# Kernel optimization log

Hardware: AMD Instinct MI355X
Metric: run time of the kernel (lower is better)

The kernel has to match this reference:

```python
import jax, jax.numpy as jnp
import numpy as np

EPS = 1e-12  # matches torch F.normalize eps

def _l2norm(x, axis):
    n = jnp.sqrt(jnp.sum(x * x, axis=axis, keepdims=True))
    return x / jnp.maximum(n, EPS)

def setup_inputs() -> dict:
    key = jax.random.key(0)
    b, N, c, h, w = 8, 4, 256, 64, 64
    n, hw, L = N - 1, h * w, 2048
    k1, k2, k3, k4, k5 = jax.random.split(key, 5)
    feat = jax.random.normal(k1, (b, c, h, w), dtype=jnp.float32)
    refs = jax.random.normal(k2, (b, N, c, h, w), dtype=jnp.float32)
    similarity = jax.random.uniform(k3, (b, N), dtype=jnp.float32)
    # unique indices per row (the torch code pads by repeating mask indices; we use
    # unique ones so the final scatter is deterministic)
    base_indices = jax.vmap(lambda k: jax.random.permutation(k, hw))(jax.random.split(k4, b))[:, :L].astype(jnp.int64)
    ref_idx = jax.vmap(lambda k: jax.random.permutation(k, hw))(jax.random.split(k5, b * n))
    ref_indices_in = ref_idx.reshape(b, n, hw)[:, :, :L].astype(jnp.int64)
    return {"feat": feat, "refs": refs, "similarity": similarity,
            "base_indices": base_indices, "ref_indices_in": ref_indices_in, "index": 0}

def reference(feat, refs, similarity, base_indices, ref_indices_in, index):
    b, N, c, h, w = refs.shape
    n, hw = N - 1, h * w
    L = base_indices.shape[1]
    # drop the base reference slot
    refs_r = jnp.concatenate([refs[:, :index], refs[:, index + 1:]], axis=1)      # [b,n,c,h,w]
    base_sim = similarity[:, index]                                              # [b]
    ref_sims = jnp.concatenate([similarity[:, :index], similarity[:, index + 1:]], axis=1)  # [b,n]

    feat_flat = feat.reshape(b, c, hw)                                           # [b,c,hw]
    w_feat = _l2norm(feat_flat.transpose(0, 2, 1), axis=2)                       # [b,hw,c]
    w_refs = _l2norm(refs_r.reshape(b, n, c, hw), axis=2)                        # [b,n,c,hw]

    # gather masked positions
    feat_select = jnp.take_along_axis(feat_flat, base_indices[:, None, :], axis=2)      # [b,c,L]
    w_feat_sel = _l2norm(jnp.take_along_axis(w_feat, base_indices[:, :, None], axis=1), axis=2)  # [b,L,c]
    w_ref_sel = jnp.take_along_axis(w_refs, ref_indices_in[:, :, None, :], axis=3)      # [b,n,c,L]

    # cosine similarity + top-1 match per base position, per reference
    fx = jnp.einsum('blc,bncm->bnlm', w_feat_sel, w_ref_sel)                     # [b,n,L,L]
    ref_indices = jnp.argmax(fx, axis=3)                                         # [b,n,L] (top-1)
    ref_selects = jnp.take_along_axis(w_ref_sel, ref_indices[:, :, None, :], axis=3)    # [b,n,c,L]

    # similarity-weighted fusion
    feat_fused = base_sim[:, None, None] * feat_select \
               + jnp.einsum('bn,bncl->bcl', ref_sims, ref_selects)               # [b,c,L]

    # scatter fused features back into the base feature map
    bi = jnp.arange(b)[:, None, None]
    ci = jnp.arange(c)[None, :, None]
    out = feat_flat.at[bi, ci, base_indices[:, None, :]].set(feat_fused)
    return out.reshape(b, c, h, w), base_indices, ref_indices
```

## Files before the change

kernel.cpp:

```cpp
#include <hip/hip_runtime.h>
#include <math.h>

#define HWp 4096
#define Cp 256
#define Lp 2048
#define Np 3
#define Bp 8

#define OUT_FEAT_N 8388608
#define OUT_BASE_OFF 8388608
#define OUT_REF_OFF 8404992
#define NROWS 49152

#define OFF_AF16  ((size_t)0)
#define OFF_BF16  ((size_t)16777216)
#define OFF_PVAL  ((size_t)117440512)
#define OFF_BEST  ((size_t)119799808)
#define OFF_CAND2 ((size_t)119996416)
#define OFF_COUNT ((size_t)120193024)
#define OFF_LIST  ((size_t)120193280)
#define OFF_INV   ((size_t)120389888)

typedef _Float16 f16x8 __attribute__((ext_vector_type(8)));
typedef float f32x4 __attribute__((ext_vector_type(4)));

__device__ __forceinline__ unsigned short f16bits(float x){
    union { _Float16 h; unsigned short s; } u;
    u.h = (_Float16)x;
    return u.s;
}

__global__ void init_inv_kernel(int4* __restrict__ inv4){
    int tid = blockIdx.x * blockDim.x + threadIdx.x;
    if (tid < 32768) inv4[tid] = make_int4(-1, -1, -1, -1);
}

__global__ void scatter_inv_kernel(const int* __restrict__ refIdxI,
                                   const int* __restrict__ baseIdx,
                                   int* __restrict__ inv){
    int tid = blockIdx.x * blockDim.x + threadIdx.x;
    if (tid < NROWS){
        int g = tid >> 11;
        inv[g*4096 + refIdxI[tid]] = tid & 2047;
    } else if (tid < NROWS + Bp*Lp){
        int t = tid - NROWS;
        int b = t >> 11;
        inv[(24 + b)*4096 + baseIdx[t]] = t & 2047;
    }
}

__global__ __launch_bounds__(256) void gather_kernel(
    const float* __restrict__ feat, const float* __restrict__ refs,
    const int* __restrict__ pindex, const int* __restrict__ inv,
    unsigned char* __restrict__ Af16, unsigned char* __restrict__ Bf16)
{
    int tileh = blockIdx.x & 127;
    int g = blockIdx.x >> 7;
    int isRef = (g < 24);
    const float* src;
    int b;
    if (isRef){
        b = g / 3; int r0 = g - b*3; int iv = *pindex;
        int rn = (r0 < iv) ? r0 : r0 + 1;
        src = refs + ((size_t)(b*4 + rn)) * Cp * HWp;
    } else {
        b = g - 24;
        src = feat + (size_t)b * Cp * HWp;
    }
    __shared__ float lds[32 * 256];
    __shared__ float ssqp[4][32];
    __shared__ float rinv[32];
    int tid = threadIdx.x, hwl = tid & 31, cg = tid >> 5;
    int hw0 = tileh * 32;
    const float* sp = src + hw0 + hwl;
    int swz = hwl << 2;
    float* lrow = lds + hwl * 256;
    float ss = 0.f;
    #pragma unroll
    for (int i = 0; i < 8; i++){
        int c0 = cg * 32 + i * 4;
        float x0 = sp[(size_t)(c0 + 0) * HWp];
        float x1 = sp[(size_t)(c0 + 1) * HWp];
        float x2 = sp[(size_t)(c0 + 2) * HWp];
        float x3 = sp[(size_t)(c0 + 3) * HWp];
        ss = fmaf(x0, x0, fmaf(x1, x1, fmaf(x2, x2, fmaf(x3, x3, ss))));
        *(float4*)(lrow + (c0 ^ swz)) = make_float4(x0, x1, x2, x3);
    }
    ss += __shfl_xor(ss, 32, 64);
    int w = tid >> 6, lane = tid & 63;
    if (lane < 32) ssqp[w][lane] = ss;
    __syncthreads();
    if (tid < 32){
        float s = ssqp[0][tid] + ssqp[1][tid] + ssqp[2][tid] + ssqp[3][tid];
        rinv[tid] = 1.0f / fmaxf(sqrtf(s), 1e-12f);
    }
    __syncthreads();
    const int* invg = inv + g * 4096 + hw0;
    unsigned char* dstBase = isRef ? (Bf16 + (size_t)g * Lp * 512)
                                   : (Af16 + (size_t)b * Lp * 512);
    for (int h = w * 8; h < w * 8 + 8; h++){
        int dest = invg[h];
        if (dest < 0) continue;
        float4 v = *(float4*)(lds + h * 256 + ((lane * 4) ^ (h << 2)));
        float rn = rinv[h];
        ushort4 hv;
        hv.x = f16bits(v.x * rn); hv.y = f16bits(v.y * rn);
        hv.z = f16bits(v.z * rn); hv.w = f16bits(v.w * rn);
        *(ushort4*)(dstBase + (size_t)dest * 512 + lane * 8) = hv;
    }
}

__device__ __forceinline__ void stage4(const unsigned char* srcLane, unsigned char* ldsW){
    #pragma unroll
    for (int p = 0; p < 4; p++)
        __builtin_amdgcn_global_load_lds(
            (const __attribute__((address_space(1))) void*)(srcLane + (p & 1) * 8192 + (p >> 1) * 64),
            (__attribute__((address_space(3))) void*)(ldsW + p * 1024),
            16, 0, 0);
}

__global__ __launch_bounds__(256, 3) void gemm_mfma_kernel(
    const unsigned char* __restrict__ Af16, const unsigned char* __restrict__ Bf16,
    unsigned int* __restrict__ ppk)
{
    int orig = (blockIdx.x & 7) * 192 + (blockIdx.x >> 3);
    int rowgrp = orig & 15;
    int chunk = (orig >> 4) % 12;
    int b = orig / 192;
    int n = chunk >> 2, c4 = chunk & 3;
    int bn = b*3 + n;
    int tid = threadIdx.x, lane = tid & 63, w = tid >> 6;
    int l15 = lane & 15, lg = lane >> 4;

    __shared__ unsigned char bufs[2][16384];

    int row0 = rowgrp*128 + w*16 + l15;
    const unsigned char* Arow0 = Af16 + ((size_t)b*Lp + row0)*512 + lg*16;
    const unsigned char* Arow1 = Arow0 + (size_t)64*512;
    f16x8 A0[8], A1[8];
    #pragma unroll
    for (int ks = 0; ks < 8; ks++){
        A0[ks] = *(const f16x8*)(Arow0 + ks*64);
        A1[ks] = *(const f16x8*)(Arow1 + ks*64);
    }

    unsigned p1[8], p2[8];
    #pragma unroll
    for (int s = 0; s < 8; s++){ p1[s] = 0u; p2[s] = 0u; }

    const unsigned char* srcLane = Bf16
        + ((size_t)(bn*2048 + c4*512)) * 512
        + l15 * 512 + (lane >> 4) * 16 + w * 128;
    unsigned char* ldsW0 = &bufs[0][w*4096];
    unsigned char* ldsW1 = &bufs[1][w*4096];

    stage4(srcLane, ldsW0);

    #pragma unroll 1
    for (int t = 0; t < 16; t++){
        if (t < 15){
            stage4(srcLane + (size_t)(t+1)*16384, (t & 1) ? ldsW0 : ldsW1);
            asm volatile("s_waitcnt vmcnt(4)" ::: "memory");
        } else {
            asm volatile("s_waitcnt vmcnt(0)" ::: "memory");
        }
        __builtin_amdgcn_s_barrier();

        const unsigned char* bp = bufs[t & 1];
        f32x4 a00 = {2.f,2.f,2.f,2.f}, a01 = {2.f,2.f,2.f,2.f};
        f32x4 a10 = {2.f,2.f,2.f,2.f}, a11 = {2.f,2.f,2.f,2.f};
        #pragma unroll
        for (int ks = 0; ks < 8; ks++){
            f16x8 b0 = *(const f16x8*)(bp + ks*2048 + lane*16);
            f16x8 b1 = *(const f16x8*)(bp + ks*2048 + 1024 + lane*16);
            a00 = __builtin_amdgcn_mfma_f32_16x16x32_f16(A0[ks], b0, a00, 0, 0, 0);
            a01 = __builtin_amdgcn_mfma_f32_16x16x32_f16(A0[ks], b1, a01, 0, 0, 0);
            a10 = __builtin_amdgcn_mfma_f32_16x16x32_f16(A1[ks], b0, a10, 0, 0, 0);
            a11 = __builtin_amdgcn_mfma_f32_16x16x32_f16(A1[ks], b1, a11, 0, 0, 0);
        }
        __builtin_amdgcn_s_barrier();

        unsigned ci0 = (unsigned)(511 - (t*32 + l15));
        unsigned ci1 = ci0 - 16;
        #pragma unroll
        for (int r = 0; r < 4; r++){
            {
                unsigned u0 = (__float_as_uint(a00[r]) & 0xFFFFFE00u) | ci0;
                unsigned u1 = (__float_as_uint(a01[r]) & 0xFFFFFE00u) | ci1;
                unsigned hi = max(u0, u1), lo = min(u0, u1);
                unsigned tm = min(p1[r], hi);
                p1[r] = max(p1[r], hi);
                p2[r] = max(p2[r], max(lo, tm));
            }
            {
                unsigned u0 = (__float_as_uint(a10[r]) & 0xFFFFFE00u) | ci0;
                unsigned u1 = (__float_as_uint(a11[r]) & 0xFFFFFE00u) | ci1;
                unsigned hi = max(u0, u1), lo = min(u0, u1);
                unsigned tm = min(p1[4+r], hi);
                p1[4+r] = max(p1[4+r], hi);
                p2[4+r] = max(p2[4+r], max(lo, tm));
            }
        }
    }

    #pragma unroll
    for (int s = 0; s < 8; s++){
        unsigned q1 = p1[s], q2 = p2[s];
        #pragma unroll
        for (int off = 1; off < 16; off <<= 1){
            unsigned o1 = (unsigned)__shfl_xor((int)q1, off, 64);
            unsigned o2 = (unsigned)__shfl_xor((int)q2, off, 64);
            unsigned m1 = max(q1, o1);
            unsigned m2 = max(min(q1, o1), max(q2, o2));
            q1 = m1; q2 = m2;
        }
        if (l15 == 0){
            int rs = s >> 2, r = s & 3;
            size_t grow = (size_t)bn*Lp + rowgrp*128 + rs*64 + w*16 + lg*4 + r;
            size_t slot = grow*4 + c4;
            ppk[slot*2 + 0] = q1;
            ppk[slot*2 + 1] = q2;
        }
    }
}

__global__ void reset_kernel(int* count){ *count = 0; }

__global__ void combine_kernel(const unsigned int* __restrict__ ppk,
                               int* __restrict__ best, int* __restrict__ cand2,
                               float* __restrict__ outF, const int* __restrict__ baseIdx,
                               int* __restrict__ count, int* __restrict__ list)
{
    int gid = blockIdx.x * blockDim.x + threadIdx.x;
    if (gid < NROWS){
        unsigned V1 = 0u, V2 = 0u; int X1 = 0, X2 = 0;
        #pragma unroll
        for (int ch = 0; ch < 4; ch++){
            unsigned u1 = ppk[((size_t)gid*4 + ch)*2 + 0];
            unsigned u2 = ppk[((size_t)gid*4 + ch)*2 + 1];
            unsigned vb1 = u1 & 0xFFFFFE00u; int c1 = ch*512 + 511 - (int)(u1 & 511u);
            unsigned vb2 = u2 & 0xFFFFFE00u; int c2 = ch*512 + 511 - (int)(u2 & 511u);
            if (vb1 > V1 || (vb1 == V1 && c1 < X1)){
                V2 = V1; X2 = X1; V1 = vb1; X1 = c1;
            } else if (vb1 > V2 || (vb1 == V2 && c1 < X2)){
                V2 = vb1; X2 = c1;
            }
            if (vb2 > V2 || (vb2 == V2 && c2 < X2)){ V2 = vb2; X2 = c2; }
        }
        best[gid] = X1; cand2[gid] = X2;
        outF[OUT_REF_OFF + gid] = (float)X1;
        if (__uint_as_float(V1) - __uint_as_float(V2) < 3.6e-4f){
            int s = atomicAdd(count, 1);
            if (s < NROWS) list[s] = gid;
        }
    }
    if (gid < Bp*Lp) outF[OUT_BASE_OFF + gid] = (float)baseIdx[gid];
}

__global__ void refine_kernel(const float* __restrict__ feat, const float* __restrict__ refs,
                              const int* __restrict__ baseIdx, const int* __restrict__ refIdxI,
                              const int* __restrict__ pindex,
                              const int* __restrict__ count, const int* __restrict__ list,
                              int* __restrict__ best, const int* __restrict__ cand2,
                              float* __restrict__ outF)
{
    int nf = *count; if (nf > NROWS) nf = NROWS;
    int lane = threadIdx.x & 63;
    int iv = *pindex;
    for (int it = blockIdx.x; it < nf; it += gridDim.x){
        int gid = list[it];
        int bn = gid >> 11, l = gid & 2047;
        int b = bn / 3; int r0 = bn - b*3;
        int rn = (r0 < iv) ? r0 : r0 + 1;
        int i1 = best[gid], i2 = cand2[gid];
        int posA = baseIdx[b*Lp + l];
        int pos1 = refIdxI[bn*Lp + i1];
        int pos2 = refIdxI[bn*Lp + i2];
        const float* fA = feat + (size_t)b * Cp * HWp + posA;
        const float* fR = refs + (size_t)(b*4 + rn) * Cp * HWp;
        const float* f1 = fR + pos1;
        const float* f2 = fR + pos2;
        double s1 = 0, s2 = 0, d1 = 0, d2 = 0;
        #pragma unroll
        for (int j = 0; j < 4; j++){
            int c = lane * 4 + j;
            double a  = (double)fA[(size_t)c * HWp];
            double x1 = (double)f1[(size_t)c * HWp];
            double x2 = (double)f2[(size_t)c * HWp];
            s1 += x1*x1; s2 += x2*x2;
            d1 += a*x1;  d2 += a*x2;
        }
        #pragma unroll
        for (int off = 1; off < 64; off <<= 1){
            s1 += __shfl_xor(s1, off, 64);
            s2 += __shfl_xor(s2, off, 64);
            d1 += __shfl_xor(d1, off, 64);
            d2 += __shfl_xor(d2, off, 64);
        }
        if (lane == 0){
            double q1 = d1 * sqrt(s2), q2 = d2 * sqrt(s1);
            int ix = (q2 > q1 || (q2 == q1 && i2 < i1)) ? i2 : i1;
            best[gid] = ix;
            outF[OUT_REF_OFF + gid] = (float)ix;
        }
    }
}

__global__ __launch_bounds__(256) void fuse_tile_kernel(
    const float* __restrict__ feat, const unsigned char* __restrict__ Bf16,
    const int* __restrict__ best, const int* __restrict__ inv,
    const float* __restrict__ sim, const int* __restrict__ pindex,
    float* __restrict__ out)
{
    int tileh = blockIdx.x & 63;
    int b = blockIdx.x >> 6;
    int hw0 = tileh * 64;
    __shared__ float lds[256 * 64];
    int tid = threadIdx.x, hwl = tid & 63, cg = tid >> 6;
    const float* fb = feat + (size_t)b * Cp * HWp + hw0 + hwl;
    #pragma unroll 4
    for (int i = 0; i < 64; i++){
        int c = cg * 64 + i;
        lds[c * 64 + ((hwl + c) & 63)] = fb[(size_t)c * HWp];
    }
    __syncthreads();
    int iv = *pindex;
    float bs  = sim[b*4 + iv];
    float rs0 = sim[b*4 + ((0 < iv) ? 0 : 1)];
    float rs1 = sim[b*4 + ((1 < iv) ? 1 : 2)];
    float rs2 = sim[b*4 + ((2 < iv) ? 2 : 3)];
    int w = cg, lane = tid & 63;
    const int* invg = inv + (24 + b) * 4096 + hw0;
    for (int h = w * 16; h < w * 16 + 16; h++){
        int dest = invg[h];
        if (dest < 0) continue;
        int b0 = best[(b*3 + 0)*Lp + dest];
        int b1 = best[(b*3 + 1)*Lp + dest];
        int b2 = best[(b*3 + 2)*Lp + dest];
        const unsigned char* r0 = Bf16 + ((size_t)(b*3 + 0)*Lp + b0) * 512;
        const unsigned char* r1 = Bf16 + ((size_t)(b*3 + 1)*Lp + b1) * 512;
        const unsigned char* r2 = Bf16 + ((size_t)(b*3 + 2)*Lp + b2) * 512;
        #pragma unroll
        for (int j = 0; j < 4; j++){
            int c = lane + j * 64;
            int la = c * 64 + ((h + c) & 63);
            float base = lds[la];
            float v0 = (float)(*(const _Float16*)(r0 + c*2));
            float v1 = (float)(*(const _Float16*)(r1 + c*2));
            float v2 = (float)(*(const _Float16*)(r2 + c*2));
            lds[la] = bs*base + rs0*v0 + rs1*v1 + rs2*v2;
        }
    }
    __syncthreads();
    float* ob = out + (size_t)b * Cp * HWp + hw0 + hwl;
    #pragma unroll 4
    for (int i = 0; i < 64; i++){
        int c = cg * 64 + i;
        ob[(size_t)c * HWp] = lds[c * 64 + ((hwl + c) & 63)];
    }
}

extern "C" void kernel_launch(void* const* d_in, const int* in_sizes, int n_in,
                              void* d_out, int out_size, void* d_ws, size_t ws_size,
                              hipStream_t stream)
{
    const float* feat    = (const float*)d_in[0];
    const float* refs    = (const float*)d_in[1];
    const float* sim     = (const float*)d_in[2];
    const int*   baseIdx = (const int*)d_in[3];
    const int*   refIdxI = (const int*)d_in[4];
    const int*   pindex  = (const int*)d_in[5];
    float* out = (float*)d_out;
    unsigned char* ws = (unsigned char*)d_ws;

    unsigned char* Af16 = ws + OFF_AF16;
    unsigned char* Bf16 = ws + OFF_BF16;
    unsigned int* ppk = (unsigned int*)(ws + OFF_PVAL);
    int* best  = (int*)(ws + OFF_BEST);
    int* cand2 = (int*)(ws + OFF_CAND2);
    int* count = (int*)(ws + OFF_COUNT);
    int* list  = (int*)(ws + OFF_LIST);
    int* inv   = (int*)(ws + OFF_INV);

    init_inv_kernel<<<128, 256, 0, stream>>>((int4*)inv);
    scatter_inv_kernel<<<256, 256, 0, stream>>>(refIdxI, baseIdx, inv);
    gather_kernel<<<4096, 256, 0, stream>>>(feat, refs, pindex, inv, Af16, Bf16);
    gemm_mfma_kernel<<<1536, 256, 0, stream>>>(Af16, Bf16, ppk);
    reset_kernel<<<1, 1, 0, stream>>>(count);
    combine_kernel<<<192, 256, 0, stream>>>(ppk, best, cand2, out, baseIdx, count, list);
    refine_kernel<<<512, 64, 0, stream>>>(feat, refs, baseIdx, refIdxI, pindex, count, list, best, cand2, out);
    fuse_tile_kernel<<<512, 256, 0, stream>>>(feat, Bf16, best, inv, sim, pindex, out);
}
```

Before: 153.3 us.

## Halve LDS staging per step to raise GEMM occupancy with split-K halves

Splits each 32-column B tile's K dimension into two half-steps, staging 8KB instead of 16KB of LDS per buffer. Launch bounds go from 3 to 6 blocks per CU. Partial accumulators from the first half are saved in registers and added to the second half before the packed top-2 update. The aim is more resident waves to hide load latency, at the cost of twice as many barriers and waits, extra live registers under a tighter register budget, and a slightly different float summation order.

```diff
diff --git a/kernel.cpp b/kernel.cpp
--- a/kernel.cpp
+++ b/kernel.cpp
@@ -110,16 +110,16 @@
     }
 }
 
-__device__ __forceinline__ void stage4(const unsigned char* srcLane, unsigned char* ldsW){
+__device__ __forceinline__ void stage2(const unsigned char* srcLane, unsigned char* ldsW){
     #pragma unroll
-    for (int p = 0; p < 4; p++)
+    for (int p = 0; p < 2; p++)
         __builtin_amdgcn_global_load_lds(
-            (const __attribute__((address_space(1))) void*)(srcLane + (p & 1) * 8192 + (p >> 1) * 64),
+            (const __attribute__((address_space(1))) void*)(srcLane + p * 8192),
             (__attribute__((address_space(3))) void*)(ldsW + p * 1024),
             16, 0, 0);
 }
 
-__global__ __launch_bounds__(256, 3) void gemm_mfma_kernel(
+__global__ __launch_bounds__(256, 6) void gemm_mfma_kernel(
     const unsigned char* __restrict__ Af16, const unsigned char* __restrict__ Bf16,
     unsigned int* __restrict__ ppk)
 {
@@ -132,7 +132,7 @@
     int tid = threadIdx.x, lane = tid & 63, w = tid >> 6;
     int l15 = lane & 15, lg = lane >> 4;
 
-    __shared__ unsigned char bufs[2][16384];
+    __shared__ unsigned char bufs[2][8192];
 
     int row0 = rowgrp*128 + w*16 + l15;
     const unsigned char* Arow0 = Af16 + ((size_t)b*Lp + row0)*512 + lg*16;
@@ -150,29 +150,33 @@
 
     const unsigned char* srcLane = Bf16
         + ((size_t)(bn*2048 + c4*512)) * 512
-        + l15 * 512 + (lane >> 4) * 16 + w * 128;
-    unsigned char* ldsW0 = &bufs[0][w*4096];
-    unsigned char* ldsW1 = &bufs[1][w*4096];
-
-    stage4(srcLane, ldsW0);
+        + l15 * 512 + (lane >> 4) * 16 + w * 64;
+
+    f32x4 sv00, sv01, sv10, sv11;
+
+    stage2(srcLane, &bufs[0][w*2048]);
 
     #pragma unroll 1
-    for (int t = 0; t < 16; t++){
-        if (t < 15){
-            stage4(srcLane + (size_t)(t+1)*16384, (t & 1) ? ldsW0 : ldsW1);
-            asm volatile("s_waitcnt vmcnt(4)" ::: "memory");
+    for (int q = 0; q < 32; q++){
+        if (q < 31){
+            int t1 = (q + 1) >> 1, h1 = (q + 1) & 1;
+            stage2(srcLane + (size_t)t1*16384 + (size_t)h1*256,
+                   &bufs[(q+1)&1][w*2048]);
+            asm volatile("s_waitcnt vmcnt(2)" ::: "memory");
         } else {
             asm volatile("s_waitcnt vmcnt(0)" ::: "memory");
         }
         __builtin_amdgcn_s_barrier();
 
-        const unsigned char* bp = bufs[t & 1];
-        f32x4 a00 = {2.f,2.f,2.f,2.f}, a01 = {2.f,2.f,2.f,2.f};
-        f32x4 a10 = {2.f,2.f,2.f,2.f}, a11 = {2.f,2.f,2.f,2.f};
-        #pragma unroll
-        for (int ks = 0; ks < 8; ks++){
-            f16x8 b0 = *(const f16x8*)(bp + ks*2048 + lane*16);
-            f16x8 b1 = *(const f16x8*)(bp + ks*2048 + 1024 + lane*16);
+        int t = q >> 1, h = q & 1;
+        const unsigned char* bp = bufs[q & 1];
+        f32x4 a00 = {0.f,0.f,0.f,0.f}, a01 = {0.f,0.f,0.f,0.f};
+        f32x4 a10 = {0.f,0.f,0.f,0.f}, a11 = {0.f,0.f,0.f,0.f};
+        #pragma unroll
+        for (int kk = 0; kk < 4; kk++){
+            f16x8 b0 = *(const f16x8*)(bp + kk*2048 + lane*16);
+            f16x8 b1 = *(const f16x8*)(bp + kk*2048 + 1024 + lane*16);
+            int ks = h*4 + kk;
             a00 = __builtin_amdgcn_mfma_f32_16x16x32_f16(A0[ks], b0, a00, 0, 0, 0);
             a01 = __builtin_amdgcn_mfma_f32_16x16x32_f16(A0[ks], b1, a01, 0, 0, 0);
             a10 = __builtin_amdgcn_mfma_f32_16x16x32_f16(A1[ks], b0, a10, 0, 0, 0);
@@ -180,25 +184,33 @@
         }
         __builtin_amdgcn_s_barrier();
 
-        unsigned ci0 = (unsigned)(511 - (t*32 + l15));
-        unsigned ci1 = ci0 - 16;
-        #pragma unroll
-        for (int r = 0; r < 4; r++){
-            {
-                unsigned u0 = (__float_as_uint(a00[r]) & 0xFFFFFE00u) | ci0;
-                unsigned u1 = (__float_as_uint(a01[r]) & 0xFFFFFE00u) | ci1;
-                unsigned hi = max(u0, u1), lo = min(u0, u1);
-                unsigned tm = min(p1[r], hi);
-                p1[r] = max(p1[r], hi);
-                p2[r] = max(p2[r], max(lo, tm));
-            }
-            {
-                unsigned u0 = (__float_as_uint(a10[r]) & 0xFFFFFE00u) | ci0;
-                unsigned u1 = (__float_as_uint(a11[r]) & 0xFFFFFE00u) | ci1;
-                unsigned hi = max(u0, u1), lo = min(u0, u1);
-                unsigned tm = min(p1[4+r], hi);
-                p1[4+r] = max(p1[4+r], hi);
-                p2[4+r] = max(p2[4+r], max(lo, tm));
+        if (h == 0){
+            sv00 = a00; sv01 = a01; sv10 = a10; sv11 = a11;
+        } else {
+            unsigned ci0 = (unsigned)(511 - (t*32 + l15));
+            unsigned ci1 = ci0 - 16;
+            #pragma unroll
+            for (int r = 0; r < 4; r++){
+                {
+                    float v0 = (sv00[r] + a00[r]) + 2.0f;
+                    float v1 = (sv01[r] + a01[r]) + 2.0f;
+                    unsigned u0 = (__float_as_uint(v0) & 0xFFFFFE00u) | ci0;
+                    unsigned u1 = (__float_as_uint(v1) & 0xFFFFFE00u) | ci1;
+                    unsigned hi = max(u0, u1), lo = min(u0, u1);
+                    unsigned tm = min(p1[r], hi);
+                    p1[r] = max(p1[r], hi);
+                    p2[r] = max(p2[r], max(lo, tm));
+                }
+                {
+                    float v0 = (sv10[r] + a10[r]) + 2.0f;
+                    float v1 = (sv11[r] + a11[r]) + 2.0f;
+                    unsigned u0 = (__float_as_uint(v0) & 0xFFFFFE00u) | ci0;
+                    unsigned u1 = (__float_as_uint(v1) & 0xFFFFFE00u) | ci1;
+                    unsigned hi = max(u0, u1), lo = min(u0, u1);
+                    unsigned tm = min(p1[4+r], hi);
+                    p1[4+r] = max(p1[4+r], hi);
+                    p2[4+r] = max(p2[4+r], max(lo, tm));
+                }
             }
         }
     }
```

Result: slower. 347.2 us (+126.4%).
